# Kernel optimization log

Measured on AMD Instinct MI355X. Metric: run time of the kernel, lower is better.

The kernel has to match this reference:

```python
import jax, jax.numpy as jnp
import numpy as np

T = 8  # number of DP iterations (self.T)

def setup_inputs() -> dict:
    key = jax.random.key(0)
    ks = jax.random.split(key, 9)
    bs, dims, L, d = 16, 4, 2048, 256
    x = jax.random.uniform(ks[0], (bs, dims, L), dtype=jnp.float32)  # one-hot-like input
    s_in = 1.0 / np.sqrt(dims)
    s_d = 1.0 / np.sqrt(d)
    W1 = jax.random.uniform(ks[1], (d, dims), minval=-s_in, maxval=s_in, dtype=jnp.float32)
    b1 = jax.random.uniform(ks[2], (d,), minval=-s_in, maxval=s_in, dtype=jnp.float32)
    W2 = jax.random.uniform(ks[3], (d, d), minval=-s_d, maxval=s_d, dtype=jnp.float32)
    b2 = jax.random.uniform(ks[4], (d,), minval=-s_d, maxval=s_d, dtype=jnp.float32)
    W3 = jax.random.uniform(ks[5], (d, dims), minval=-s_in, maxval=s_in, dtype=jnp.float32)
    b3 = jax.random.uniform(ks[6], (d,), minval=-s_in, maxval=s_in, dtype=jnp.float32)
    W4 = jax.random.uniform(ks[7], (d, d), minval=-s_d, maxval=s_d, dtype=jnp.float32)
    b4 = jax.random.uniform(ks[8], (d,), minval=-s_d, maxval=s_d, dtype=jnp.float32)
    return dict(x=x, W1=W1, b1=b1, W2=W2, b2=b2, W3=W3, b3=b3, W4=W4, b4=b4)

def reference(x, W1, b1, W2, b2, W3, b3, W4, b4):
    # x: (bs, dims, L). The original allocates V:(bs,T+1,L+2,L+2,d) but only the
    # two diagonals V[i,j,j+1] ("up") and V[i,j,j-1] ("down") are ever written/read,
    # so the recurrence collapses to two (bs,L,d) lanes.
    a = jnp.einsum('bdl,od->blo', x, W1) + b1  # W1(x_j) for all j: (bs, L, d)
    bs, L, d = a.shape
    zcol = jnp.zeros((bs, 1, d), a.dtype)
    shift_r = lambda v: jnp.concatenate([zcol, v[:, :-1]], axis=1)  # v[j-1], zero at j=0
    shift_l = lambda v: jnp.concatenate([v[:, 1:], zcol], axis=1)   # v[j+1], zero at j=L-1
    up = jnp.zeros_like(a)   # up[j]   = V[i, j+1, j+2] (0-indexed lane)
    down = jnp.zeros_like(a) # down[j] = V[i, j+1, j]
    for _ in range(T):
        up = jax.nn.relu(a + shift_r(up) @ W2.T + b2)
        down = jax.nn.relu(a + shift_l(down) @ W2.T + b2)
    c = jnp.einsum('bdl,od->blo', x, W3) + b3
    # miu[j] = relu(W3 x_j + W4(V[T,j-1,j]) + W4(V[T,j+1,j]))
    miu = jax.nn.relu(c + (shift_r(up) @ W4.T + b4) + (shift_l(down) @ W4.T + b4))
    return miu  # (bs, L, d)
```

## Files before the change

### kernel.cpp

```cpp
#include <hip/hip_runtime.h>


typedef __bf16 bf16x8 __attribute__((ext_vector_type(8)));
typedef __bf16 bf16x4 __attribute__((ext_vector_type(4)));
typedef float f32x16 __attribute__((ext_vector_type(16)));
typedef unsigned int uint2v __attribute__((ext_vector_type(2)));

#define MFMA32(a, b, c) __builtin_amdgcn_mfma_f32_32x32x16_bf16(a, b, c, 0, 0, 0)

__device__ __forceinline__ unsigned short f2bf(float f) {
  unsigned int u = __builtin_bit_cast(unsigned int, f);
  u += 0x7fffu + ((u >> 16) & 1u);
  return (unsigned short)(u >> 16);
}

__global__ void prep_kernel(const float* __restrict__ W1, const float* __restrict__ b1,
                            const float* __restrict__ W2, const float* __restrict__ b2,
                            const float* __restrict__ W3, const float* __restrict__ b3,
                            const float* __restrict__ W4, const float* __restrict__ b4,
                            unsigned short* __restrict__ ws) {
  int idx = blockIdx.x * 256 + threadIdx.x;
  if (idx >= 139264) return;
  float v = 0.0f;
  if (idx < 131072) {
    const float* W = (idx < 65536) ? W2 : W4;
    int i = idx & 65535;
    int j = i & 7, f = i >> 3;
    int lane = f & 63, slot = f >> 6;
    int ks = slot & 15, ot = slot >> 4;
    int o = ot * 32 + (lane & 31);
    int k = ks * 16 + (lane >> 5) * 8 + j;
    v = W[o * 256 + k];
  } else {
    int i = idx - 131072;
    bool first = (i < 4096);
    int ii = i & 4095;
    int j = ii & 7, f = ii >> 3;
    int lane = f & 63, ot = f >> 6;
    int o = ot * 32 + (lane & 31);
    if (lane < 32) {
      if (j < 4) v = first ? W1[o * 4 + j] : W3[o * 4 + j];
      else if (j == 4) v = first ? (b1[o] + b2[o]) : (b3[o] + 2.0f * b4[o]);
    }
  }
  ws[idx] = f2bf(v);
}

#define GSTEP(RB, KS) { \
    bf16x8 bu_ = __builtin_bit_cast(bf16x8, (RB)[(2 * (KS) + khalf) * 32 + lane31]); \
    acc[0] = MFMA32(w2c[0][KS], bu_, acc[0]); \
    acc[1] = MFMA32(w2c[1][KS], bu_, acc[1]); }

#define PACKWRITE(WB) { \
    _Pragma("unroll") for (int t2 = 0; t2 < 2; ++t2) { \
      unsigned lo[4], hi[4]; \
      _Pragma("unroll") for (int q = 0; q < 4; ++q) { \
        bf16x4 h; \
        h.x = (__bf16)fmaxf(acc[t2][4 * q + 0], 0.0f); \
        h.y = (__bf16)fmaxf(acc[t2][4 * q + 1], 0.0f); \
        h.z = (__bf16)fmaxf(acc[t2][4 * q + 2], 0.0f); \
        h.w = (__bf16)fmaxf(acc[t2][4 * q + 3], 0.0f); \
        uint2 u = __builtin_bit_cast(uint2, h); \
        lo[q] = u.x; hi[q] = u.y; \
      } \
      uint2v r0 = __builtin_amdgcn_permlane32_swap(lo[0], lo[1], false, false); \
      uint2v r1 = __builtin_amdgcn_permlane32_swap(hi[0], hi[1], false, false); \
      (WB)[((ot0 + t2) * 4 + khalf) * 32 + lane31] = \
          make_int4((int)r0.x, (int)r1.x, (int)r0.y, (int)r1.y); \
      uint2v r2 = __builtin_amdgcn_permlane32_swap(lo[2], lo[3], false, false); \
      uint2v r3 = __builtin_amdgcn_permlane32_swap(hi[2], hi[3], false, false); \
      (WB)[((ot0 + t2) * 4 + 2 + khalf) * 32 + lane31] = \
          make_int4((int)r2.x, (int)r3.x, (int)r2.y, (int)r3.y); \
    } }

#define INTERVAL(PH, T, RB, WB, DOG) { \
  f32x16 acc[2] = {}; \
  { int widx = (PH) == 0 ? (lane31 + (T) - 1) : (lane31 + 17 - (T)); \
    const int4* p_ = (l < 32) ? (xw + widx) : (&zc); \
    bf16x8 bx_ = __builtin_bit_cast(bf16x8, *p_); \
    acc[0] = MFMA32(w1x[0], bx_, acc[0]); \
    acc[1] = MFMA32(w1x[1], bx_, acc[1]); } \
  if (DOG) { \
    __builtin_amdgcn_s_setprio(1); \
    GSTEP(RB, 0)  GSTEP(RB, 1)  GSTEP(RB, 2)  GSTEP(RB, 3) \
    GSTEP(RB, 4)  GSTEP(RB, 5)  GSTEP(RB, 6)  GSTEP(RB, 7) \
    GSTEP(RB, 8)  GSTEP(RB, 9)  GSTEP(RB, 10) GSTEP(RB, 11) \
    GSTEP(RB, 12) GSTEP(RB, 13) GSTEP(RB, 14) GSTEP(RB, 15) \
    __builtin_amdgcn_s_setprio(0); \
  } \
  PACKWRITE(WB) }

__global__ __launch_bounds__(256, 2)
void chain_kernel(const float* __restrict__ x, const unsigned short* __restrict__ ws,
                  float* __restrict__ out) {
  __shared__ int4 UA[2][1024];
  __shared__ int4 UB[2][1024];
  __shared__ int4 xw[48];
  __shared__ int4 zc;

  const int tid = threadIdx.x;
  const int l = tid & 63;
  const int w = tid >> 6;
  const int lane31 = l & 31;
  const int khalf = l >> 5;
  const int tile = blockIdx.x;
  const int b = tile >> 6;
  const int j0 = (tile & 63) * 32;

  const int4* w2f = (const int4*)ws;
  const int4* w4f = (const int4*)(ws + 65536);
  const int4* w1xg = (const int4*)(ws + 131072);
  const int4* w3xg = (const int4*)(ws + 135168);

  if (tid == 0) zc = make_int4(0, 0, 0, 0);
  if (tid < 48) {
    int j = j0 - 8 + tid;
    int4 c = make_int4(0, 0, 0, 0);
    if (j >= 0 && j < 2048) {
      const float* xb = x + (b * 4) * 2048 + j;
      unsigned short h0 = f2bf(xb[0]);
      unsigned short h1 = f2bf(xb[2048]);
      unsigned short h2 = f2bf(xb[4096]);
      unsigned short h3 = f2bf(xb[6144]);
      c = make_int4((int)(h0 | ((unsigned int)h1 << 16)),
                    (int)(h2 | ((unsigned int)h3 << 16)),
                    0x00003f80, 0);
    }
    xw[tid] = c;
  }

  const int ot0 = w * 2;
  bf16x8 w2c[2][16];
  bf16x8 w1x[2];
#pragma unroll
  for (int t2 = 0; t2 < 2; ++t2) {
    w1x[t2] = __builtin_bit_cast(bf16x8, w1xg[(ot0 + t2) * 64 + l]);
#pragma unroll
    for (int i = 0; i < 16; ++i)
      w2c[t2][i] = __builtin_bit_cast(bf16x8, w2f[((ot0 + t2) * 16 + i) * 64 + l]);
  }
  __syncthreads();

  INTERVAL(0, 1, UA[0], UA[0], false)
  INTERVAL(1, 1, UB[0], UB[0], false)
  __syncthreads();

#pragma unroll 1
  for (int k = 1; k < 8; ++k) {
    const int4* ra = UA[(k - 1) & 1];
    int4* wa = UA[k & 1];
    const int4* rb = UB[(k - 1) & 1];
    int4* wb = UB[k & 1];
    const int T = k + 1;
    INTERVAL(0, T, ra, wa, true)
    INTERVAL(1, T, rb, wb, true)
    __syncthreads();
  }

  {
    f32x16 acc[2] = {};
    { int widx = lane31 + 8;
      const int4* p_ = (l < 32) ? (xw + widx) : (&zc);
      bf16x8 bx = __builtin_bit_cast(bf16x8, *p_);
      bf16x8 w3x0 = __builtin_bit_cast(bf16x8, w3xg[ot0 * 64 + l]);
      bf16x8 w3x1 = __builtin_bit_cast(bf16x8, w3xg[(ot0 + 1) * 64 + l]);
      acc[0] = MFMA32(w3x0, bx, acc[0]);
      acc[1] = MFMA32(w3x1, bx, acc[1]); }
    __builtin_amdgcn_s_setprio(1);
#pragma unroll 1
    for (int ph = 0; ph < 2; ++ph) {
      const int4* Sp = ph ? UB[1] : UA[1];
#pragma unroll
      for (int ks = 0; ks < 16; ++ks) {
        bf16x8 af0 = __builtin_bit_cast(bf16x8, w4f[(ot0 * 16 + ks) * 64 + l]);
        bf16x8 af1 = __builtin_bit_cast(bf16x8, w4f[((ot0 + 1) * 16 + ks) * 64 + l]);
        bf16x8 bu = __builtin_bit_cast(bf16x8, Sp[(2 * ks + khalf) * 32 + lane31]);
        acc[0] = MFMA32(af0, bu, acc[0]);
        acc[1] = MFMA32(af1, bu, acc[1]);
      }
    }
    __builtin_amdgcn_s_setprio(0);
    int pbase = (b * 2048 + j0 + lane31) * 256;
#pragma unroll
    for (int t2 = 0; t2 < 2; ++t2) {
#pragma unroll
      for (int q = 0; q < 4; ++q) {
        int ob = (ot0 + t2) * 32 + 8 * q + 4 * khalf;
        float4 v;
        v.x = fmaxf(acc[t2][4 * q + 0], 0.0f);
        v.y = fmaxf(acc[t2][4 * q + 1], 0.0f);
        v.z = fmaxf(acc[t2][4 * q + 2], 0.0f);
        v.w = fmaxf(acc[t2][4 * q + 3], 0.0f);
        *(float4*)(out + pbase + ob) = v;
      }
    }
  }
}

extern "C" void kernel_launch(void* const* d_in, const int* in_sizes, int n_in,
                              void* d_out, int out_size, void* d_ws, size_t ws_size,
                              hipStream_t stream) {
  const float* x  = (const float*)d_in[0];
  const float* W1 = (const float*)d_in[1];
  const float* b1 = (const float*)d_in[2];
  const float* W2 = (const float*)d_in[3];
  const float* b2 = (const float*)d_in[4];
  const float* W3 = (const float*)d_in[5];
  const float* b3 = (const float*)d_in[6];
  const float* W4 = (const float*)d_in[7];
  const float* b4 = (const float*)d_in[8];
  unsigned short* ws = (unsigned short*)d_ws;

  prep_kernel<<<544, 256, 0, stream>>>(W1, b1, W2, b2, W3, b3, W4, b4, ws);
  chain_kernel<<<1024, 256, 0, stream>>>(x, ws, (float*)d_out);
}
```

Measured before the change: 134.7 us.

## Keep own-wave hidden slice in registers, cache partial W2, vectorize prep

Each wave now keeps the four K-slices of the hidden state it produced in registers and uses them directly for its own MFMA steps, reading only the other slices from shared memory. K-steps are rotated per wave. Only 10 of the 16 W2 fragments stay resident in registers; the other 6 are streamed from global/L2 inside each iteration, which lowers register pressure. The final W4 stage reuses the register-held slices as well, and the prep kernel is vectorized to write 8 bf16 values per thread. The extra global loads in the hot loop may add latency.

```diff
diff --git a/kernel.cpp b/kernel.cpp
--- a/kernel.cpp
+++ b/kernel.cpp
@@ -12,6 +12,10 @@
   unsigned int u = __builtin_bit_cast(unsigned int, f);
   u += 0x7fffu + ((u >> 16) & 1u);
   return (unsigned short)(u >> 16);
+}
+
+__device__ __forceinline__ unsigned pk2(float a, float b) {
+  return (unsigned)f2bf(a) | ((unsigned)f2bf(b) << 16);
 }
 
 __global__ void prep_kernel(const float* __restrict__ W1, const float* __restrict__ b1,
@@ -19,39 +23,60 @@
                             const float* __restrict__ W3, const float* __restrict__ b3,
                             const float* __restrict__ W4, const float* __restrict__ b4,
                             unsigned short* __restrict__ ws) {
-  int idx = blockIdx.x * 256 + threadIdx.x;
-  if (idx >= 139264) return;
-  float v = 0.0f;
+  int t8 = blockIdx.x * 256 + threadIdx.x;
+  if (t8 >= 17408) return;
+  int idx = t8 * 8;
+  int4 outv;
   if (idx < 131072) {
     const float* W = (idx < 65536) ? W2 : W4;
-    int i = idx & 65535;
-    int j = i & 7, f = i >> 3;
+    int f = (idx & 65535) >> 3;
     int lane = f & 63, slot = f >> 6;
     int ks = slot & 15, ot = slot >> 4;
     int o = ot * 32 + (lane & 31);
-    int k = ks * 16 + (lane >> 5) * 8 + j;
-    v = W[o * 256 + k];
+    int kbase = ks * 16 + (lane >> 5) * 8;
+    const float4* row = (const float4*)(W + o * 256 + kbase);
+    float4 v0 = row[0];
+    float4 v1 = row[1];
+    outv = make_int4((int)pk2(v0.x, v0.y), (int)pk2(v0.z, v0.w),
+                     (int)pk2(v1.x, v1.y), (int)pk2(v1.z, v1.w));
   } else {
     int i = idx - 131072;
     bool first = (i < 4096);
-    int ii = i & 4095;
-    int j = ii & 7, f = ii >> 3;
+    int f = (i & 4095) >> 3;
     int lane = f & 63, ot = f >> 6;
     int o = ot * 32 + (lane & 31);
+    outv = make_int4(0, 0, 0, 0);
     if (lane < 32) {
-      if (j < 4) v = first ? W1[o * 4 + j] : W3[o * 4 + j];
-      else if (j == 4) v = first ? (b1[o] + b2[o]) : (b3[o] + 2.0f * b4[o]);
-    }
-  }
-  ws[idx] = f2bf(v);
-}
-
-#define GSTEP(RB, KS) { \
-    bf16x8 bu_ = __builtin_bit_cast(bf16x8, (RB)[(2 * (KS) + khalf) * 32 + lane31]); \
-    acc[0] = MFMA32(w2c[0][KS], bu_, acc[0]); \
-    acc[1] = MFMA32(w2c[1][KS], bu_, acc[1]); }
-
-#define PACKWRITE(WB) { \
+      const float4 wrow = *(const float4*)((first ? W1 : W3) + o * 4);
+      float bias = first ? (b1[o] + b2[o]) : (b3[o] + 2.0f * b4[o]);
+      outv = make_int4((int)pk2(wrow.x, wrow.y), (int)pk2(wrow.z, wrow.w),
+                       (int)pk2(bias, 0.0f), 0);
+    }
+  }
+  *(int4*)(ws + idx) = outv;
+}
+
+#define NC 10
+
+#define LOAD_AF(AF, S0) { \
+    int ka_ = (4 * w + NC + (S0)) & 15; \
+    AF[0][0] = __builtin_bit_cast(bf16x8, w2f[(ot0 * 16 + ka_) * 64 + l]); \
+    AF[0][1] = __builtin_bit_cast(bf16x8, w2f[((ot0 + 1) * 16 + ka_) * 64 + l]); \
+    int kb_ = (4 * w + NC + (S0) + 1) & 15; \
+    AF[1][0] = __builtin_bit_cast(bf16x8, w2f[(ot0 * 16 + kb_) * 64 + l]); \
+    AF[1][1] = __builtin_bit_cast(bf16x8, w2f[((ot0 + 1) * 16 + kb_) * 64 + l]); }
+
+#define GSTEP(RB, KSR, A0, A1) { \
+    bf16x8 bu_ = __builtin_bit_cast(bf16x8, (RB)[(2 * (KSR) + khalf) * 32 + lane31]); \
+    acc[0] = MFMA32(A0, bu_, acc[0]); \
+    acc[1] = MFMA32(A1, bu_, acc[1]); }
+
+#define SELFSTEP(ZK, S) { \
+    bf16x8 bu_ = __builtin_bit_cast(bf16x8, ZK[(S) >> 1][(S) & 1]); \
+    acc[0] = MFMA32(w2c[0][S], bu_, acc[0]); \
+    acc[1] = MFMA32(w2c[1][S], bu_, acc[1]); }
+
+#define PACKZ(ZK) { \
     _Pragma("unroll") for (int t2 = 0; t2 < 2; ++t2) { \
       unsigned lo[4], hi[4]; \
       _Pragma("unroll") for (int q = 0; q < 4; ++q) { \
@@ -65,30 +90,54 @@
       } \
       uint2v r0 = __builtin_amdgcn_permlane32_swap(lo[0], lo[1], false, false); \
       uint2v r1 = __builtin_amdgcn_permlane32_swap(hi[0], hi[1], false, false); \
-      (WB)[((ot0 + t2) * 4 + khalf) * 32 + lane31] = \
-          make_int4((int)r0.x, (int)r1.x, (int)r0.y, (int)r1.y); \
+      ZK[t2][0] = make_int4((int)r0.x, (int)r1.x, (int)r0.y, (int)r1.y); \
       uint2v r2 = __builtin_amdgcn_permlane32_swap(lo[2], lo[3], false, false); \
       uint2v r3 = __builtin_amdgcn_permlane32_swap(hi[2], hi[3], false, false); \
-      (WB)[((ot0 + t2) * 4 + 2 + khalf) * 32 + lane31] = \
-          make_int4((int)r2.x, (int)r3.x, (int)r2.y, (int)r3.y); \
+      ZK[t2][1] = make_int4((int)r2.x, (int)r3.x, (int)r2.y, (int)r3.y); \
     } }
 
-#define INTERVAL(PH, T, RB, WB, DOG) { \
-  f32x16 acc[2] = {}; \
-  { int widx = (PH) == 0 ? (lane31 + (T) - 1) : (lane31 + 17 - (T)); \
-    const int4* p_ = (l < 32) ? (xw + widx) : (&zc); \
+#define WRITEZ(ZK, WB) { \
+    _Pragma("unroll") for (int t2 = 0; t2 < 2; ++t2) \
+    _Pragma("unroll") for (int p = 0; p < 2; ++p) \
+      (WB)[((ot0 + t2) * 4 + 2 * p + khalf) * 32 + lane31] = ZK[t2][p]; }
+
+#define XWSTEP(PH, T) { \
+    int widx_ = (PH) == 0 ? (lane31 + (T) - 1) : (lane31 + 17 - (T)); \
+    const int4* p_ = (l < 32) ? (xw + widx_) : (&zc); \
     bf16x8 bx_ = __builtin_bit_cast(bf16x8, *p_); \
     acc[0] = MFMA32(w1x[0], bx_, acc[0]); \
-    acc[1] = MFMA32(w1x[1], bx_, acc[1]); } \
-  if (DOG) { \
-    __builtin_amdgcn_s_setprio(1); \
-    GSTEP(RB, 0)  GSTEP(RB, 1)  GSTEP(RB, 2)  GSTEP(RB, 3) \
-    GSTEP(RB, 4)  GSTEP(RB, 5)  GSTEP(RB, 6)  GSTEP(RB, 7) \
-    GSTEP(RB, 8)  GSTEP(RB, 9)  GSTEP(RB, 10) GSTEP(RB, 11) \
-    GSTEP(RB, 12) GSTEP(RB, 13) GSTEP(RB, 14) GSTEP(RB, 15) \
-    __builtin_amdgcn_s_setprio(0); \
-  } \
-  PACKWRITE(WB) }
+    acc[1] = MFMA32(w1x[1], bx_, acc[1]); }
+
+#define INTERVAL_G(PH, T, RB, WB, ZK) { \
+  bf16x8 afA[2][2], afB[2][2], afC[2][2]; \
+  LOAD_AF(afA, 0) \
+  f32x16 acc[2] = {}; \
+  XWSTEP(PH, T) \
+  __builtin_amdgcn_s_setprio(1); \
+  SELFSTEP(ZK, 0) SELFSTEP(ZK, 1) SELFSTEP(ZK, 2) SELFSTEP(ZK, 3) \
+  LOAD_AF(afB, 2) \
+  GSTEP(RB, (4 * w + 4) & 15, w2c[0][4], w2c[1][4]) \
+  GSTEP(RB, (4 * w + 5) & 15, w2c[0][5], w2c[1][5]) \
+  GSTEP(RB, (4 * w + 6) & 15, w2c[0][6], w2c[1][6]) \
+  GSTEP(RB, (4 * w + 7) & 15, w2c[0][7], w2c[1][7]) \
+  GSTEP(RB, (4 * w + 8) & 15, w2c[0][8], w2c[1][8]) \
+  GSTEP(RB, (4 * w + 9) & 15, w2c[0][9], w2c[1][9]) \
+  GSTEP(RB, (4 * w + 10) & 15, afA[0][0], afA[0][1]) \
+  GSTEP(RB, (4 * w + 11) & 15, afA[1][0], afA[1][1]) \
+  LOAD_AF(afC, 4) \
+  GSTEP(RB, (4 * w + 12) & 15, afB[0][0], afB[0][1]) \
+  GSTEP(RB, (4 * w + 13) & 15, afB[1][0], afB[1][1]) \
+  GSTEP(RB, (4 * w + 14) & 15, afC[0][0], afC[0][1]) \
+  GSTEP(RB, (4 * w + 15) & 15, afC[1][0], afC[1][1]) \
+  __builtin_amdgcn_s_setprio(0); \
+  PACKZ(ZK) \
+  WRITEZ(ZK, WB) }
+
+#define INTERVAL_P(PH, WB, ZK) { \
+  f32x16 acc[2] = {}; \
+  XWSTEP(PH, 1) \
+  PACKZ(ZK) \
+  WRITEZ(ZK, WB) }
 
 __global__ __launch_bounds__(256, 2)
 void chain_kernel(const float* __restrict__ x, const unsigned short* __restrict__ ws,
@@ -130,19 +179,23 @@
   }
 
   const int ot0 = w * 2;
-  bf16x8 w2c[2][16];
+  bf16x8 w2c[2][NC];
   bf16x8 w1x[2];
 #pragma unroll
   for (int t2 = 0; t2 < 2; ++t2) {
     w1x[t2] = __builtin_bit_cast(bf16x8, w1xg[(ot0 + t2) * 64 + l]);
 #pragma unroll
-    for (int i = 0; i < 16; ++i)
-      w2c[t2][i] = __builtin_bit_cast(bf16x8, w2f[((ot0 + t2) * 16 + i) * 64 + l]);
+    for (int i = 0; i < NC; ++i) {
+      int ksr = (4 * w + i) & 15;
+      w2c[t2][i] = __builtin_bit_cast(bf16x8, w2f[((ot0 + t2) * 16 + ksr) * 64 + l]);
+    }
   }
   __syncthreads();
 
-  INTERVAL(0, 1, UA[0], UA[0], false)
-  INTERVAL(1, 1, UB[0], UB[0], false)
+  int4 zkU[2][2], zkD[2][2];
+
+  INTERVAL_P(0, UA[0], zkU)
+  INTERVAL_P(1, UB[0], zkD)
   __syncthreads();
 
 #pragma unroll 1
@@ -152,8 +205,8 @@
     const int4* rb = UB[(k - 1) & 1];
     int4* wb = UB[k & 1];
     const int T = k + 1;
-    INTERVAL(0, T, ra, wa, true)
-    INTERVAL(1, T, rb, wb, true)
+    INTERVAL_G(0, T, ra, wa, zkU)
+    INTERVAL_G(1, T, rb, wb, zkD)
     __syncthreads();
   }
 
@@ -170,11 +223,22 @@
 #pragma unroll 1
     for (int ph = 0; ph < 2; ++ph) {
       const int4* Sp = ph ? UB[1] : UA[1];
-#pragma unroll
-      for (int ks = 0; ks < 16; ++ks) {
-        bf16x8 af0 = __builtin_bit_cast(bf16x8, w4f[(ot0 * 16 + ks) * 64 + l]);
-        bf16x8 af1 = __builtin_bit_cast(bf16x8, w4f[((ot0 + 1) * 16 + ks) * 64 + l]);
-        bf16x8 bu = __builtin_bit_cast(bf16x8, Sp[(2 * ks + khalf) * 32 + lane31]);
+      const int4* zz = ph ? &zkD[0][0] : &zkU[0][0];
+#pragma unroll
+      for (int s = 0; s < 4; ++s) {
+        int ksr = 4 * w + s;
+        bf16x8 af0 = __builtin_bit_cast(bf16x8, w4f[(ot0 * 16 + ksr) * 64 + l]);
+        bf16x8 af1 = __builtin_bit_cast(bf16x8, w4f[((ot0 + 1) * 16 + ksr) * 64 + l]);
+        bf16x8 bu = __builtin_bit_cast(bf16x8, zz[s]);
+        acc[0] = MFMA32(af0, bu, acc[0]);
+        acc[1] = MFMA32(af1, bu, acc[1]);
+      }
+#pragma unroll
+      for (int i = 4; i < 16; ++i) {
+        int ksr = (4 * w + i) & 15;
+        bf16x8 af0 = __builtin_bit_cast(bf16x8, w4f[(ot0 * 16 + ksr) * 64 + l]);
+        bf16x8 af1 = __builtin_bit_cast(bf16x8, w4f[((ot0 + 1) * 16 + ksr) * 64 + l]);
+        bf16x8 bu = __builtin_bit_cast(bf16x8, Sp[(2 * ksr + khalf) * 32 + lane31]);
         acc[0] = MFMA32(af0, bu, acc[0]);
         acc[1] = MFMA32(af1, bu, acc[1]);
       }
@@ -211,6 +275,6 @@
   const float* b4 = (const float*)d_in[8];
   unsigned short* ws = (unsigned short*)d_ws;
 
-  prep_kernel<<<544, 256, 0, stream>>>(W1, b1, W2, b2, W3, b3, W4, b4, ws);
+  prep_kernel<<<68, 256, 0, stream>>>(W1, b1, W2, b2, W3, b3, W4, b4, ws);
   chain_kernel<<<1024, 256, 0, stream>>>(x, ws, (float*)d_out);
 }
```

New measurement: 128.5 us (median of 2 runs). 4.6% less time.
